# Kernel optimization log

Measured on AMD Instinct MI355X. Metric: run time of the kernel, lower is better.

## Reference

```python
import jax, jax.numpy as jnp
import numpy as np

WINDOWS = [7, 15, 31, 63, 127]
MAX_W = max(WINDOWS)
PAD = MAX_W // 2 + 1  # 64, matches K.spatial_2d_padding amount
HALF = MAX_W // 2     # 63


def _sat(a):
    """Integral image (summed-area table) of zero-padded input, per original layer."""
    ap = jnp.pad(a, ((0, 0), (PAD, PAD), (PAD, PAD), (0, 0)))
    return jnp.cumsum(jnp.cumsum(ap, axis=1), axis=2)


def _multi_window_means(a):
    """Box means for all window sizes. a: [B,H,W,C] -> [B,n_wins,H,W,C].
    Computes the count SAT once (original redundantly recomputes it per window;
    math is identical)."""
    B, H, W, C = a.shape
    ii = _sat(a)
    cnt_ii = _sat(jnp.ones_like(a[:1, ..., :1]))  # [1, H+2P, W+2P, 1]

    def box(ii_, h, w):
        top = HALF - h // 2
        left = HALF - w // 2
        bot, right = top + h, left + w
        return (ii_[:, top:top + H, left:left + W]
                + ii_[:, bot:bot + H, right:right + W]
                - ii_[:, top:top + H, right:right + W]
                - ii_[:, bot:bot + H, left:left + W])

    means = [box(ii, h, h) / box(cnt_ii, h, h) for h in WINDOWS]
    return jnp.stack(means, axis=1)  # [B, n_wins, H, W, C]


def setup_inputs() -> dict:
    key = jax.random.key(0)
    k1, _ = jax.random.split(key)
    B, H, W, C = 8, 1024, 1024, 1
    n_wins = len(WINDOWS)
    x = jax.random.uniform(k1, (B, H, W, C), dtype=jnp.float32)  # normalized image in (0,1)
    k = jnp.full((1, n_wins, 1, 1, 1), 0.2, dtype=jnp.float32)   # init_k
    R = jnp.full((1, n_wins, 1, 1, 1), 0.5, dtype=jnp.float32)   # init_R
    return {"x": x, "k": k, "R": R}


def reference(x, k, R):
    E_x = _multi_window_means(x)          # [B,5,H,W,C]
    E_x2 = _multi_window_means(x * x)
    dev_x = jnp.sqrt(jnp.maximum(E_x2 - E_x * E_x, 1e-6))
    T = E_x * (1.0 + k * (dev_x / R - 1.0))
    return T.astype(jnp.float32)
```

## Files before the change

### kernel.cpp

```cpp
#include <hip/hip_runtime.h>
#include <cstddef>

#define B_ 8
#define H_ 1024
#define W_ 1024
#define NW_ 5
#define CHUNKS_ 32
#define CHROWS_ (H_ / CHUNKS_)

__global__ __launch_bounds__(256) void k_rowpart(const float* __restrict__ x,
                                                 float* __restrict__ P1,
                                                 float* __restrict__ P2,
                                                 float* __restrict__ part1,
                                                 float* __restrict__ part2) {
  const int ch = blockIdx.x, b = blockIdx.y;
  const int wave = threadIdx.x >> 6, lane = threadIdx.x & 63;
  const int row0 = ch * CHROWS_ + wave * (CHROWS_ / 4);

  float4 acc1[4], acc2[4];
  #pragma unroll
  for (int c = 0; c < 4; ++c) {
    acc1[c] = make_float4(0.f, 0.f, 0.f, 0.f);
    acc2[c] = make_float4(0.f, 0.f, 0.f, 0.f);
  }

  for (int rr = 0; rr < CHROWS_ / 4; ++rr) {
    const int y = row0 + rr;
    const size_t rowoff = ((size_t)b * H_ + y) * W_;
    float carry1 = 0.f, carry2 = 0.f;
    #pragma unroll
    for (int c = 0; c < 4; ++c) {
      const float4 v = reinterpret_cast<const float4*>(x + rowoff + c * 256)[lane];
      float l1[4], l2[4];
      l1[0] = v.x - 0.5f;
      l1[1] = l1[0] + (v.y - 0.5f);
      l1[2] = l1[1] + (v.z - 0.5f);
      l1[3] = l1[2] + (v.w - 0.5f);
      l2[0] = v.x * v.x - (1.0f / 3.0f);
      l2[1] = l2[0] + (v.y * v.y - (1.0f / 3.0f));
      l2[2] = l2[1] + (v.z * v.z - (1.0f / 3.0f));
      l2[3] = l2[2] + (v.w * v.w - (1.0f / 3.0f));
      const float s1 = l1[3], s2 = l2[3];
      float inc1 = s1, inc2 = s2;
      #pragma unroll
      for (int off = 1; off < 64; off <<= 1) {
        const float t1 = __shfl_up(inc1, off);
        const float t2 = __shfl_up(inc2, off);
        if (lane >= off) { inc1 += t1; inc2 += t2; }
      }
      const float base1 = carry1 + inc1 - s1;
      const float base2 = carry2 + inc2 - s2;
      float4 o1, o2;
      o1.x = base1 + l1[0]; o1.y = base1 + l1[1]; o1.z = base1 + l1[2]; o1.w = base1 + l1[3];
      o2.x = base2 + l2[0]; o2.y = base2 + l2[1]; o2.z = base2 + l2[2]; o2.w = base2 + l2[3];
      reinterpret_cast<float4*>(P1 + rowoff + c * 256)[lane] = o1;
      reinterpret_cast<float4*>(P2 + rowoff + c * 256)[lane] = o2;
      acc1[c].x += o1.x; acc1[c].y += o1.y; acc1[c].z += o1.z; acc1[c].w += o1.w;
      acc2[c].x += o2.x; acc2[c].y += o2.y; acc2[c].z += o2.z; acc2[c].w += o2.w;
      carry1 += __shfl(inc1, 63);
      carry2 += __shfl(inc2, 63);
    }
  }

  __shared__ float red[4][2][W_];
  #pragma unroll
  for (int c = 0; c < 4; ++c) {
    reinterpret_cast<float4*>(&red[wave][0][c * 256])[lane] = acc1[c];
    reinterpret_cast<float4*>(&red[wave][1][c * 256])[lane] = acc2[c];
  }
  __syncthreads();
  const int t = threadIdx.x;
  float4 r1 = make_float4(0.f, 0.f, 0.f, 0.f), r2 = r1;
  #pragma unroll
  for (int w = 0; w < 4; ++w) {
    const float4 a = reinterpret_cast<const float4*>(&red[w][0][0])[t];
    const float4 c2 = reinterpret_cast<const float4*>(&red[w][1][0])[t];
    r1.x += a.x; r1.y += a.y; r1.z += a.z; r1.w += a.w;
    r2.x += c2.x; r2.y += c2.y; r2.z += c2.z; r2.w += c2.w;
  }
  const size_t po = ((size_t)(b * CHUNKS_ + ch)) * W_;
  reinterpret_cast<float4*>(part1 + po)[t] = r1;
  reinterpret_cast<float4*>(part2 + po)[t] = r2;
}

__global__ __launch_bounds__(256) void k_colscan(float* __restrict__ P1,
                                                 float* __restrict__ P2,
                                                 const float* __restrict__ part1,
                                                 const float* __restrict__ part2) {
  const int xx = blockIdx.x * 256 + threadIdx.x;
  const int ch = blockIdx.y, b = blockIdx.z;
  float r1 = 0.f, r2 = 0.f;
  for (int c = 0; c < ch; ++c) {
    const size_t o = ((size_t)(b * CHUNKS_ + c)) * W_ + xx;
    r1 += part1[o];
    r2 += part2[o];
  }
  float* p1 = P1 + ((size_t)b * H_ + (size_t)ch * CHROWS_) * W_ + xx;
  float* p2 = P2 + ((size_t)b * H_ + (size_t)ch * CHROWS_) * W_ + xx;
  #pragma unroll 8
  for (int i = 0; i < CHROWS_; ++i) {
    const size_t o = (size_t)i * W_;
    r1 += p1[o]; p1[o] = r1;
    r2 += p2[o]; p2[o] = r2;
  }
}

__global__ __launch_bounds__(256) void k_out(const float* __restrict__ S1,
                                             const float* __restrict__ S2,
                                             const float* __restrict__ kk,
                                             const float* __restrict__ RR,
                                             float* __restrict__ out) {
  const int i = blockIdx.x;
  const int xcd = i & 7;
  const int s = i >> 3;
  const int b = s >> 7;
  const int y = xcd * 128 + (s & 127);
  const int t = threadIdx.x;

  __shared__ float lds[2 * NW_ * W_];

  const float* base1 = S1 + (size_t)b * H_ * W_;
  const float* base2 = S2 + (size_t)b * H_ * W_;
  const int rad[NW_] = {3, 7, 15, 31, 63};

  #pragma unroll
  for (int w = 0; w < NW_; ++w) {
    const int r = rad[w];
    const int yB = min(y + r, H_ - 1);
    const int yT = y - r - 1;
    const float4 fb1 = reinterpret_cast<const float4*>(base1 + (size_t)yB * W_)[t];
    const float4 fb2 = reinterpret_cast<const float4*>(base2 + (size_t)yB * W_)[t];
    float4 ft1 = {0.f, 0.f, 0.f, 0.f}, ft2 = {0.f, 0.f, 0.f, 0.f};
    if (yT >= 0) {
      ft1 = reinterpret_cast<const float4*>(base1 + (size_t)yT * W_)[t];
      ft2 = reinterpret_cast<const float4*>(base2 + (size_t)yT * W_)[t];
    }
    float4 d1, d2;
    d1.x = fb1.x - ft1.x; d1.y = fb1.y - ft1.y; d1.z = fb1.z - ft1.z; d1.w = fb1.w - ft1.w;
    d2.x = fb2.x - ft2.x; d2.y = fb2.y - ft2.y; d2.z = fb2.z - ft2.z; d2.w = fb2.w - ft2.w;
    reinterpret_cast<float4*>(lds + (size_t)(2 * w) * W_)[t] = d1;
    reinterpret_cast<float4*>(lds + (size_t)(2 * w + 1) * W_)[t] = d2;
  }
  __syncthreads();

  #pragma unroll
  for (int w = 0; w < NW_; ++w) {
    const int r = rad[w];
    const float kw = kk[w];
    const float invR = __builtin_amdgcn_rcpf(RR[w]);
    const int yB = min(y + r, H_ - 1);
    const float rows = (float)(yB - max(y - r, 0) + 1);
    const float* D1 = lds + (size_t)(2 * w) * W_;
    const float* D2 = lds + (size_t)(2 * w + 1) * W_;
    float* orow = out + (((size_t)(b * NW_ + w)) * H_ + y) * W_;
    #pragma unroll
    for (int kp = 0; kp < 4; ++kp) {
      const int xx = t + kp * 256;
      const int xR = min(xx + r, W_ - 1);
      const int xL = xx - r - 1;
      float s1 = D1[xR];
      float s2 = D2[xR];
      if (xL >= 0) { s1 -= D1[xL]; s2 -= D2[xL]; }
      const float cols = (float)(xR - max(xx - r, 0) + 1);
      const float inv = __builtin_amdgcn_rcpf(rows * cols);
      const float Ex  = s1 * inv + 0.5f;
      const float Ex2 = s2 * inv + (1.0f / 3.0f);
      const float var = Ex2 - Ex * Ex;
      const float dev = __builtin_amdgcn_sqrtf(fmaxf(var, 1e-6f));
      orow[xx] = Ex * (1.0f + kw * (dev * invR - 1.0f));
    }
  }
}

extern "C" void kernel_launch(void* const* d_in, const int* in_sizes, int n_in,
                              void* d_out, int out_size, void* d_ws, size_t ws_size,
                              hipStream_t stream) {
  const float* x  = (const float*)d_in[0];
  const float* kk = (const float*)d_in[1];
  const float* RR = (const float*)d_in[2];
  float* out = (float*)d_out;

  const size_t plane = (size_t)B_ * H_ * W_;
  float* P1 = (float*)d_ws;
  float* P2 = P1 + plane;
  float* part1 = P2 + plane;
  float* part2 = part1 + (size_t)B_ * CHUNKS_ * W_;

  k_rowpart <<<dim3(CHUNKS_, B_),          256, 0, stream>>>(x, P1, P2, part1, part2);
  k_colscan <<<dim3(W_/256, CHUNKS_, B_),  256, 0, stream>>>(P1, P2, part1, part2);
  k_out     <<<dim3(B_ * H_),              256, 0, stream>>>(P1, P2, kk, RR, out);
}
```

Measured before the change: 249.0 us.

## Fuse local column scan into row pass and defer chunk prefixes to output kernel

```diff
diff --git a/kernel.cpp b/kernel.cpp
--- a/kernel.cpp
+++ b/kernel.cpp
@@ -5,17 +5,17 @@
 #define H_ 1024
 #define W_ 1024
 #define NW_ 5
-#define CHUNKS_ 32
-#define CHROWS_ (H_ / CHUNKS_)
+#define CH_ 4
+#define NCH_ (H_ / CH_)
 
 __global__ __launch_bounds__(256) void k_rowpart(const float* __restrict__ x,
                                                  float* __restrict__ P1,
                                                  float* __restrict__ P2,
                                                  float* __restrict__ part1,
                                                  float* __restrict__ part2) {
-  const int ch = blockIdx.x, b = blockIdx.y;
+  const int b = blockIdx.y;
   const int wave = threadIdx.x >> 6, lane = threadIdx.x & 63;
-  const int row0 = ch * CHROWS_ + wave * (CHROWS_ / 4);
+  const int y0 = blockIdx.x * 16 + wave * CH_;
 
   float4 acc1[4], acc2[4];
   #pragma unroll
@@ -24,8 +24,9 @@
     acc2[c] = make_float4(0.f, 0.f, 0.f, 0.f);
   }
 
-  for (int rr = 0; rr < CHROWS_ / 4; ++rr) {
-    const int y = row0 + rr;
+  #pragma unroll
+  for (int rr = 0; rr < CH_; ++rr) {
+    const int y = y0 + rr;
     const size_t rowoff = ((size_t)b * H_ + y) * W_;
     float carry1 = 0.f, carry2 = 0.f;
     #pragma unroll
@@ -50,63 +51,44 @@
       }
       const float base1 = carry1 + inc1 - s1;
       const float base2 = carry2 + inc2 - s2;
-      float4 o1, o2;
-      o1.x = base1 + l1[0]; o1.y = base1 + l1[1]; o1.z = base1 + l1[2]; o1.w = base1 + l1[3];
-      o2.x = base2 + l2[0]; o2.y = base2 + l2[1]; o2.z = base2 + l2[2]; o2.w = base2 + l2[3];
-      reinterpret_cast<float4*>(P1 + rowoff + c * 256)[lane] = o1;
-      reinterpret_cast<float4*>(P2 + rowoff + c * 256)[lane] = o2;
-      acc1[c].x += o1.x; acc1[c].y += o1.y; acc1[c].z += o1.z; acc1[c].w += o1.w;
-      acc2[c].x += o2.x; acc2[c].y += o2.y; acc2[c].z += o2.z; acc2[c].w += o2.w;
+      acc1[c].x += base1 + l1[0]; acc1[c].y += base1 + l1[1];
+      acc1[c].z += base1 + l1[2]; acc1[c].w += base1 + l1[3];
+      acc2[c].x += base2 + l2[0]; acc2[c].y += base2 + l2[1];
+      acc2[c].z += base2 + l2[2]; acc2[c].w += base2 + l2[3];
+      reinterpret_cast<float4*>(P1 + rowoff + c * 256)[lane] = acc1[c];
+      reinterpret_cast<float4*>(P2 + rowoff + c * 256)[lane] = acc2[c];
       carry1 += __shfl(inc1, 63);
       carry2 += __shfl(inc2, 63);
     }
   }
 
-  __shared__ float red[4][2][W_];
+  const int cc = y0 >> 2;
+  const size_t po = ((size_t)(b * NCH_ + cc)) * W_;
   #pragma unroll
   for (int c = 0; c < 4; ++c) {
-    reinterpret_cast<float4*>(&red[wave][0][c * 256])[lane] = acc1[c];
-    reinterpret_cast<float4*>(&red[wave][1][c * 256])[lane] = acc2[c];
+    reinterpret_cast<float4*>(part1 + po + c * 256)[lane] = acc1[c];
+    reinterpret_cast<float4*>(part2 + po + c * 256)[lane] = acc2[c];
   }
-  __syncthreads();
-  const int t = threadIdx.x;
-  float4 r1 = make_float4(0.f, 0.f, 0.f, 0.f), r2 = r1;
-  #pragma unroll
-  for (int w = 0; w < 4; ++w) {
-    const float4 a = reinterpret_cast<const float4*>(&red[w][0][0])[t];
-    const float4 c2 = reinterpret_cast<const float4*>(&red[w][1][0])[t];
-    r1.x += a.x; r1.y += a.y; r1.z += a.z; r1.w += a.w;
-    r2.x += c2.x; r2.y += c2.y; r2.z += c2.z; r2.w += c2.w;
-  }
-  const size_t po = ((size_t)(b * CHUNKS_ + ch)) * W_;
-  reinterpret_cast<float4*>(part1 + po)[t] = r1;
-  reinterpret_cast<float4*>(part2 + po)[t] = r2;
 }
 
-__global__ __launch_bounds__(256) void k_colscan(float* __restrict__ P1,
-                                                 float* __restrict__ P2,
-                                                 const float* __restrict__ part1,
-                                                 const float* __restrict__ part2) {
+__global__ __launch_bounds__(256) void k_ppscan(float* __restrict__ part1,
+                                                float* __restrict__ part2) {
   const int xx = blockIdx.x * 256 + threadIdx.x;
-  const int ch = blockIdx.y, b = blockIdx.z;
+  const int b = blockIdx.y;
   float r1 = 0.f, r2 = 0.f;
-  for (int c = 0; c < ch; ++c) {
-    const size_t o = ((size_t)(b * CHUNKS_ + c)) * W_ + xx;
-    r1 += part1[o];
-    r2 += part2[o];
-  }
-  float* p1 = P1 + ((size_t)b * H_ + (size_t)ch * CHROWS_) * W_ + xx;
-  float* p2 = P2 + ((size_t)b * H_ + (size_t)ch * CHROWS_) * W_ + xx;
   #pragma unroll 8
-  for (int i = 0; i < CHROWS_; ++i) {
-    const size_t o = (size_t)i * W_;
-    r1 += p1[o]; p1[o] = r1;
-    r2 += p2[o]; p2[o] = r2;
+  for (int c = 0; c < NCH_; ++c) {
+    const size_t o = ((size_t)(b * NCH_ + c)) * W_ + xx;
+    const float t1 = part1[o], t2 = part2[o];
+    part1[o] = r1; part2[o] = r2;
+    r1 += t1; r2 += t2;
   }
 }
 
 __global__ __launch_bounds__(256) void k_out(const float* __restrict__ S1,
                                              const float* __restrict__ S2,
+                                             const float* __restrict__ pp1,
+                                             const float* __restrict__ pp2,
                                              const float* __restrict__ kk,
                                              const float* __restrict__ RR,
                                              float* __restrict__ out) {
@@ -121,19 +103,31 @@
 
   const float* base1 = S1 + (size_t)b * H_ * W_;
   const float* base2 = S2 + (size_t)b * H_ * W_;
+  const float* pb1 = pp1 + (size_t)b * NCH_ * W_;
+  const float* pb2 = pp2 + (size_t)b * NCH_ * W_;
   const int rad[NW_] = {3, 7, 15, 31, 63};
 
   #pragma unroll
   for (int w = 0; w < NW_; ++w) {
     const int r = rad[w];
     const int yB = min(y + r, H_ - 1);
+    const int ccB = yB >> 2;
+    float4 fb1 = reinterpret_cast<const float4*>(base1 + (size_t)yB * W_)[t];
+    float4 fb2 = reinterpret_cast<const float4*>(base2 + (size_t)yB * W_)[t];
+    const float4 qb1 = reinterpret_cast<const float4*>(pb1 + (size_t)ccB * W_)[t];
+    const float4 qb2 = reinterpret_cast<const float4*>(pb2 + (size_t)ccB * W_)[t];
+    fb1.x += qb1.x; fb1.y += qb1.y; fb1.z += qb1.z; fb1.w += qb1.w;
+    fb2.x += qb2.x; fb2.y += qb2.y; fb2.z += qb2.z; fb2.w += qb2.w;
+    float4 ft1 = {0.f, 0.f, 0.f, 0.f}, ft2 = {0.f, 0.f, 0.f, 0.f};
     const int yT = y - r - 1;
-    const float4 fb1 = reinterpret_cast<const float4*>(base1 + (size_t)yB * W_)[t];
-    const float4 fb2 = reinterpret_cast<const float4*>(base2 + (size_t)yB * W_)[t];
-    float4 ft1 = {0.f, 0.f, 0.f, 0.f}, ft2 = {0.f, 0.f, 0.f, 0.f};
     if (yT >= 0) {
+      const int ccT = yT >> 2;
       ft1 = reinterpret_cast<const float4*>(base1 + (size_t)yT * W_)[t];
       ft2 = reinterpret_cast<const float4*>(base2 + (size_t)yT * W_)[t];
+      const float4 qt1 = reinterpret_cast<const float4*>(pb1 + (size_t)ccT * W_)[t];
+      const float4 qt2 = reinterpret_cast<const float4*>(pb2 + (size_t)ccT * W_)[t];
+      ft1.x += qt1.x; ft1.y += qt1.y; ft1.z += qt1.z; ft1.w += qt1.w;
+      ft2.x += qt2.x; ft2.y += qt2.y; ft2.z += qt2.z; ft2.w += qt2.w;
     }
     float4 d1, d2;
     d1.x = fb1.x - ft1.x; d1.y = fb1.y - ft1.y; d1.z = fb1.z - ft1.z; d1.w = fb1.w - ft1.w;
@@ -184,9 +178,9 @@
   float* P1 = (float*)d_ws;
   float* P2 = P1 + plane;
   float* part1 = P2 + plane;
-  float* part2 = part1 + (size_t)B_ * CHUNKS_ * W_;
+  float* part2 = part1 + (size_t)B_ * NCH_ * W_;
 
-  k_rowpart <<<dim3(CHUNKS_, B_),          256, 0, stream>>>(x, P1, P2, part1, part2);
-  k_colscan <<<dim3(W_/256, CHUNKS_, B_),  256, 0, stream>>>(P1, P2, part1, part2);
-  k_out     <<<dim3(B_ * H_),              256, 0, stream>>>(P1, P2, kk, RR, out);
+  k_rowpart <<<dim3(H_ / 16, B_),   256, 0, stream>>>(x, P1, P2, part1, part2);
+  k_ppscan  <<<dim3(W_ / 256, B_),  256, 0, stream>>>(part1, part2);
+  k_out     <<<dim3(B_ * H_),       256, 0, stream>>>(P1, P2, part1, part2, kk, RR, out);
 }
```

Measured after the change: 269.6 us. +8.3%, slower.
